# Performance work log

Hardware: AMD Instinct MI355X
Metric: run time of the kernel (lower is better)

The kernel has to match this reference:

```python
import jax, jax.numpy as jnp
import numpy as np

N = 65536      # total nodes = B * MAXN
E = 524288     # edges (avg degree 8)
DX = 32; DG = 32
IN_DIM = DX + 3 * DG   # 128, after concat(x, g0, g1, g2)
H = 256; OUT = 8; MAXN = 8192


def setup_inputs() -> dict:
    key = jax.random.key(0)
    ks = jax.random.split(key, 40)
    inp = {}
    inp['x'] = jax.random.normal(ks[0], (N, DX), jnp.float32)
    inp['g0'] = jax.random.normal(ks[1], (N, DG), jnp.float32)
    inp['g1'] = jax.random.normal(ks[2], (N, DG), jnp.float32)
    inp['g2'] = jax.random.normal(ks[3], (N, DG), jnp.float32)
    inp['edge_src'] = jax.random.randint(ks[4], (E,), 0, N, jnp.int32)
    inp['edge_dst'] = jax.random.randint(ks[5], (E,), 0, N, jnp.int32)
    dims = [(IN_DIM, H), (H, H), (H, H), (H, H)]
    k = 6
    for i, (di, do) in enumerate(dims):
        s = 1.0 / np.sqrt(di)
        inp[f'Wl{i}'] = jax.random.uniform(ks[k], (di, do), jnp.float32, -s, s); k += 1
        inp[f'Wr{i}'] = jax.random.uniform(ks[k], (di, do), jnp.float32, -s, s); k += 1
        inp[f'b{i}'] = jnp.zeros((do,), jnp.float32)
    s = 1.0 / np.sqrt(MAXN)
    inp['mlp1_W1'] = jax.random.uniform(ks[k], (MAXN, H), jnp.float32, -s, s); k += 1
    inp['mlp1_b1'] = jnp.zeros((H,), jnp.float32)
    s = 1.0 / np.sqrt(H)
    inp['mlp1_W2'] = jax.random.uniform(ks[k], (H, 1), jnp.float32, -s, s); k += 1
    inp['mlp1_b2'] = jnp.zeros((1,), jnp.float32)
    inp['bn_gamma'] = jnp.ones((H,), jnp.float32)
    inp['bn_beta'] = jnp.zeros((H,), jnp.float32)
    inp['mlp2_W1'] = jax.random.uniform(ks[k], (H, H), jnp.float32, -s, s); k += 1
    inp['mlp2_b1'] = jnp.zeros((H,), jnp.float32)
    inp['mlp2_W2'] = jax.random.uniform(ks[k], (H, OUT), jnp.float32, -s, s); k += 1
    inp['mlp2_b2'] = jnp.zeros((OUT,), jnp.float32)
    return inp


def _forward(x, g0, g1, g2, edge_src, edge_dst,
             Wl0, Wr0, b0, Wl1, Wr1, b1, Wl2, Wr2, b2, Wl3, Wr3, b3,
             mlp1_W1, mlp1_b1, mlp1_W2, mlp1_b2, bn_gamma, bn_beta,
             mlp2_W1, mlp2_b1, mlp2_W2, mlp2_b2):
    h = jnp.concatenate([x, g0, g1, g2], axis=1)  # [N, IN_DIM]
    # mean-aggregation denominator (in-degree, clamped at 1 like PyG mean)
    cnt = jnp.maximum(
        jax.ops.segment_sum(jnp.ones((E,), h.dtype), edge_dst, num_segments=N), 1.0)
    for Wl, Wr, b in ((Wl0, Wr0, b0), (Wl1, Wr1, b1), (Wl2, Wr2, b2), (Wl3, Wr3, b3)):
        agg = jax.ops.segment_sum(h[edge_src], edge_dst, num_segments=N) / cnt[:, None]
        # SAGEConv: lin_l(mean of neighbors) + lin_r(self) + bias, then ReLU
        h = jax.nn.relu(agg @ Wl + h @ Wr + b)
        # F.dropout in eval / deterministic reference: identity
    h = h.reshape(-1, H, MAXN)                               # [B, H, MAXN]
    h = jax.nn.relu(jnp.einsum('bhm,mk->bhk', h, mlp1_W1) + mlp1_b1)
    h = (jnp.einsum('bhk,ko->bho', h, mlp1_W2) + mlp1_b2)[..., 0]  # [B, H]
    mean = h.mean(axis=0)
    var = h.var(axis=0)
    h = (h - mean) / jnp.sqrt(var + 1e-5) * bn_gamma + bn_beta
    h = jax.nn.relu(h)
    h = jax.nn.relu(h @ mlp2_W1 + mlp2_b1)
    return h @ mlp2_W2 + mlp2_b2                              # [B, OUT]


def reference(x, g0, g1, g2, edge_src, edge_dst,
              Wl0, Wr0, b0, Wl1, Wr1, b1, Wl2, Wr2, b2, Wl3, Wr3, b3,
              mlp1_W1, mlp1_b1, mlp1_W2, mlp1_b2, bn_gamma, bn_beta,
              mlp2_W1, mlp2_b1, mlp2_W2, mlp2_b2):
    return _forward(x, g0, g1, g2, edge_src, edge_dst,
                    Wl0, Wr0, b0, Wl1, Wr1, b1, Wl2, Wr2, b2, Wl3, Wr3, b3,
                    mlp1_W1, mlp1_b1, mlp1_W2, mlp1_b2, bn_gamma, bn_beta,
                    mlp2_W1, mlp2_b1, mlp2_W2, mlp2_b2)
```

## Files before the change

### kernel.cpp

```cpp
#include <hip/hip_runtime.h>
#include <hip/hip_bf16.h>


#define NN 65536
#define EE 524288
#define ROWS 65537
#define PCSR_CAP 720896

using frag16 = __attribute__((ext_vector_type(8))) short;
using f32x4  = __attribute__((ext_vector_type(4))) float;

__device__ __forceinline__ float b2f(unsigned short u) {
    union { unsigned u32; float f; } x; x.u32 = (unsigned)u << 16; return x.f;
}

__device__ __forceinline__ unsigned short f2b(float f) {
    return (unsigned short)(__bfloat16_as_ushort(__float2bfloat16(f)));
}

__device__ __forceinline__ void gld_lds16(const void* g, void* l) {
    __builtin_amdgcn_global_load_lds(
        (const __attribute__((address_space(1))) void*)g,
        (__attribute__((address_space(3))) void*)l, 16, 0, 0);
}


__global__ void gs_zero_deg(int* deg) {
    int i = blockIdx.x * 256 + threadIdx.x;
    if (i < NN) deg[i] = 0;
}

__global__ void gs_hist(const int* __restrict__ dst, int* __restrict__ deg) {
    int e = blockIdx.x * 256 + threadIdx.x;
    atomicAdd(&deg[dst[e]], 1);
}

__global__ void gs_deg_reduce(const int* __restrict__ deg, int* __restrict__ bsum) {
    int t = threadIdx.x;
    int p = (deg[blockIdx.x * 256 + t] + 3) & ~3;
#pragma unroll
    for (int off = 32; off > 0; off >>= 1) p += __shfl_down(p, off);
    __shared__ int w4[4];
    if ((t & 63) == 0) w4[t >> 6] = p;
    __syncthreads();
    if (t == 0) bsum[blockIdx.x] = w4[0] + w4[1] + w4[2] + w4[3];
}

__global__ void gs_scan_bsum(const int* __restrict__ bsum, int* __restrict__ bofs,
                             int* __restrict__ prow) {
    __shared__ int part[256];
    int t = threadIdx.x;
    int v = bsum[t];
    part[t] = v;
    __syncthreads();
    for (int off = 1; off < 256; off <<= 1) {
        int add = (t >= off) ? part[t - off] : 0;
        __syncthreads();
        part[t] += add;
        __syncthreads();
    }
    bofs[t] = part[t] - v;
    if (t == 255) prow[NN] = part[255];
}

__global__ void gs_scan_apply(const int* __restrict__ deg, const int* __restrict__ bofs,
                              int* __restrict__ prow, int* __restrict__ cursor,
                              float* __restrict__ inv_cnt, int* __restrict__ pcsr,
                              __hip_bfloat16* __restrict__ P0,
                              __hip_bfloat16* __restrict__ P1) {
    __shared__ int part[256];
    int t = threadIdx.x;
    int i = blockIdx.x * 256 + t;
    int d = deg[i];
    int p = (d + 3) & ~3;
    part[t] = p;
    __syncthreads();
    for (int off = 1; off < 256; off <<= 1) {
        int add = (t >= off) ? part[t - off] : 0;
        __syncthreads();
        part[t] += add;
        __syncthreads();
    }
    int beg = bofs[blockIdx.x] + part[t] - p;
    prow[i] = beg;
    cursor[i] = beg;
    inv_cnt[i] = 1.0f / (float)(d > 0 ? d : 1);
    for (int j = d; j < p; ++j) pcsr[beg + j] = NN;
    if (blockIdx.x == 0) {
        ((unsigned*)(P0 + (size_t)NN * 512))[t] = 0u;
        ((unsigned*)(P1 + (size_t)NN * 512))[t] = 0u;
    }
}

__global__ void gs_bucket(const int* __restrict__ src, const int* __restrict__ dst,
                          int* __restrict__ cursor, int* __restrict__ pcsr) {
    int e = blockIdx.x * 256 + threadIdx.x;
    int d = dst[e];
    int p = atomicAdd(&cursor[d], 1);
    pcsr[p] = src[e];
}

struct TcvtArgs {
    const float* src[8];
    __hip_bfloat16* dst[8];
    int ldk[8];
    int kofs[8];
    int kblk[8];
};

__global__ void gs_tcvt_all(TcvtArgs a) {
    int z = blockIdx.z;
    if ((int)blockIdx.x >= a.kblk[z]) return;
    const float* src = a.src[z];
    __hip_bfloat16* dst = a.dst[z];
    int ldk = a.ldk[z], kofs = a.kofs[z];
    __shared__ float tile[32][33];
    int kb = blockIdx.x * 32, nb = blockIdx.y * 32;
    int tx = threadIdx.x, ty = threadIdx.y;
#pragma unroll
    for (int i = 0; i < 32; i += 8)
        tile[ty + i][tx] = src[(size_t)(kb + ty + i) * 256 + nb + tx];
    __syncthreads();
#pragma unroll
    for (int i = 0; i < 32; i += 8) {
        int n = nb + ty + i, k = kb + tx;
        dst[(size_t)n * ldk + kofs + k] = __float2bfloat16(tile[tx][ty + i]);
    }
}

__global__ void gs_tcvt(const float* __restrict__ src, __hip_bfloat16* __restrict__ dst,
                        int ldk, int kofs) {
    __shared__ float tile[32][33];
    int kb = blockIdx.x * 32, nb = blockIdx.y * 32;
    int tx = threadIdx.x, ty = threadIdx.y;
#pragma unroll
    for (int i = 0; i < 32; i += 8)
        tile[ty + i][tx] = src[(size_t)(kb + ty + i) * 256 + nb + tx];
    __syncthreads();
#pragma unroll
    for (int i = 0; i < 32; i += 8) {
        int n = nb + ty + i, k = kb + tx;
        dst[(size_t)n * ldk + kofs + k] = __float2bfloat16(tile[tx][ty + i]);
    }
}

__global__ void gs_concat_bf(const float* __restrict__ x, const float* __restrict__ g0,
                             const float* __restrict__ g1, const float* __restrict__ g2,
                             __hip_bfloat16* __restrict__ h) {
    int idx = blockIdx.x * 256 + threadIdx.x;
    int n = idx >> 7, c = idx & 127;
    float v;
    if (c < 32)       v = x[n * 32 + c];
    else if (c < 64)  v = g0[n * 32 + (c - 32)];
    else if (c < 96)  v = g1[n * 32 + (c - 64)];
    else              v = g2[n * 32 + (c - 96)];
    h[(size_t)n * 512 + 256 + c] = __float2bfloat16(v);
}

template <int DIM>
__global__ void gs_agg_bf(const __hip_bfloat16* __restrict__ hsrc,
                          __hip_bfloat16* __restrict__ adst,
                          const int* __restrict__ prow, const int* __restrict__ pcsr,
                          const float* __restrict__ inv_cnt) {
    int wave = threadIdx.x >> 6;
    int lane = threadIdx.x & 63;
    int n = blockIdx.x * 4 + wave;
    int e = prow[n], pe = prow[n + 1];
    float iv = inv_cnt[n];
    if constexpr (DIM == 256) {
        const __hip_bfloat16* base = hsrc + lane * 4;
        float a0 = 0.f, a1 = 0.f, a2 = 0.f, a3 = 0.f;
        while (e < pe) {
            int4 ia = *(const int4*)(pcsr + e);
            int4 ib;
            if (e + 4 < pe) ib = *(const int4*)(pcsr + e + 4);
            else            ib = make_int4(NN, NN, NN, NN);
            e += 8;
            ushort4 v0 = *(const ushort4*)(base + (size_t)ia.x * 512);
            ushort4 v1 = *(const ushort4*)(base + (size_t)ia.y * 512);
            ushort4 v2 = *(const ushort4*)(base + (size_t)ia.z * 512);
            ushort4 v3 = *(const ushort4*)(base + (size_t)ia.w * 512);
            ushort4 v4 = *(const ushort4*)(base + (size_t)ib.x * 512);
            ushort4 v5 = *(const ushort4*)(base + (size_t)ib.y * 512);
            ushort4 v6 = *(const ushort4*)(base + (size_t)ib.z * 512);
            ushort4 v7 = *(const ushort4*)(base + (size_t)ib.w * 512);
            a0 += b2f(v0.x); a1 += b2f(v0.y); a2 += b2f(v0.z); a3 += b2f(v0.w);
            a0 += b2f(v1.x); a1 += b2f(v1.y); a2 += b2f(v1.z); a3 += b2f(v1.w);
            a0 += b2f(v2.x); a1 += b2f(v2.y); a2 += b2f(v2.z); a3 += b2f(v2.w);
            a0 += b2f(v3.x); a1 += b2f(v3.y); a2 += b2f(v3.z); a3 += b2f(v3.w);
            a0 += b2f(v4.x); a1 += b2f(v4.y); a2 += b2f(v4.z); a3 += b2f(v4.w);
            a0 += b2f(v5.x); a1 += b2f(v5.y); a2 += b2f(v5.z); a3 += b2f(v5.w);
            a0 += b2f(v6.x); a1 += b2f(v6.y); a2 += b2f(v6.z); a3 += b2f(v6.w);
            a0 += b2f(v7.x); a1 += b2f(v7.y); a2 += b2f(v7.z); a3 += b2f(v7.w);
        }
        __hip_bfloat16 o[4] = {__float2bfloat16(a0 * iv), __float2bfloat16(a1 * iv),
                               __float2bfloat16(a2 * iv), __float2bfloat16(a3 * iv)};
        *(ushort4*)(adst + (size_t)n * 512 + lane * 4) = *(const ushort4*)o;
    } else {
        const __hip_bfloat16* base = hsrc + lane * 2;
        float a0 = 0.f, a1 = 0.f;
        while (e < pe) {
            int4 ia = *(const int4*)(pcsr + e);
            int4 ib;
            if (e + 4 < pe) ib = *(const int4*)(pcsr + e + 4);
            else            ib = make_int4(NN, NN, NN, NN);
            e += 8;
            ushort2 v0 = *(const ushort2*)(base + (size_t)ia.x * 512);
            ushort2 v1 = *(const ushort2*)(base + (size_t)ia.y * 512);
            ushort2 v2 = *(const ushort2*)(base + (size_t)ia.z * 512);
            ushort2 v3 = *(const ushort2*)(base + (size_t)ia.w * 512);
            ushort2 v4 = *(const ushort2*)(base + (size_t)ib.x * 512);
            ushort2 v5 = *(const ushort2*)(base + (size_t)ib.y * 512);
            ushort2 v6 = *(const ushort2*)(base + (size_t)ib.z * 512);
            ushort2 v7 = *(const ushort2*)(base + (size_t)ib.w * 512);
            a0 += b2f(v0.x); a1 += b2f(v0.y);
            a0 += b2f(v1.x); a1 += b2f(v1.y);
            a0 += b2f(v2.x); a1 += b2f(v2.y);
            a0 += b2f(v3.x); a1 += b2f(v3.y);
            a0 += b2f(v4.x); a1 += b2f(v4.y);
            a0 += b2f(v5.x); a1 += b2f(v5.y);
            a0 += b2f(v6.x); a1 += b2f(v6.y);
            a0 += b2f(v7.x); a1 += b2f(v7.y);
        }
        __hip_bfloat16 o[2] = {__float2bfloat16(a0 * iv), __float2bfloat16(a1 * iv)};
        *(ushort2*)(adst + (size_t)n * 512 + lane * 2) = *(const ushort2*)o;
    }
}

__device__ __forceinline__ void mfma_block(const __hip_bfloat16* A, int lda,
                                           const __hip_bfloat16* Bt, int ldb,
                                           int kbeg, int kend, size_t row0, size_t nbase,
                                           __hip_bfloat16* As, __hip_bfloat16* Bs,
                                           f32x4 acc[4][4]) {
    const int t = threadIdx.x;
    const int lane = t & 63;
    const int w = t >> 6;
    const int wr = (w >> 1) * 64;
    const int wc = (w & 1) * 64;
    const int srow = w * 32 + (lane >> 3);
    const int scol = (lane & 7) * 8;
    for (int kc = kbeg; kc < kend; kc += 64) {
#pragma unroll
        for (int l = 0; l < 4; ++l) {
            gld_lds16(A + (row0 + srow + 8 * l) * (size_t)lda + kc + scol,
                      As + (w * 32 + 8 * l) * 64);
            gld_lds16(Bt + (nbase + srow + 8 * l) * (size_t)ldb + kc + scol,
                      Bs + (w * 32 + 8 * l) * 64);
        }
        __syncthreads();
#pragma unroll
        for (int kk = 0; kk < 64; kk += 32) {
            frag16 af[4], bf[4];
#pragma unroll
            for (int i = 0; i < 4; ++i)
                af[i] = *(const frag16*)(As + (wr + i * 16 + (lane & 15)) * 64 + kk + (lane >> 4) * 8);
#pragma unroll
            for (int j = 0; j < 4; ++j)
                bf[j] = *(const frag16*)(Bs + (wc + j * 16 + (lane & 15)) * 64 + kk + (lane >> 4) * 8);
#pragma unroll
            for (int i = 0; i < 4; ++i)
#pragma unroll
                for (int j = 0; j < 4; ++j)
                    acc[i][j] = __builtin_amdgcn_mfma_f32_16x16x32_bf16(bf[j], af[i], acc[i][j], 0, 0, 0);
        }
        __syncthreads();
    }
}

__global__ __launch_bounds__(256, 2)
void gs_gemm_bias_relu(const __hip_bfloat16* __restrict__ A, int lda, int K,
                       const __hip_bfloat16* __restrict__ Bt, int ldb,
                       const float* __restrict__ bias,
                       __hip_bfloat16* __restrict__ C, int ldc, int cofs) {
    __shared__ __hip_bfloat16 As[128 * 64];
    __shared__ __hip_bfloat16 Bs[128 * 64];
    f32x4 acc[4][4] = {};
    const size_t row0 = (size_t)blockIdx.x * 128;
    const size_t nbase = (size_t)blockIdx.y * 128;
    mfma_block(A, lda, Bt, ldb, 0, K, row0, nbase, As, Bs, acc);
    const int lane = threadIdx.x & 63;
    const int w = threadIdx.x >> 6;
    const int wr = (w >> 1) * 64, wc = (w & 1) * 64;
#pragma unroll
    for (int j = 0; j < 4; ++j) {
        int nb = wc + j * 16 + (lane >> 4) * 4;
        const float4 bv = *(const float4*)&bias[(int)nbase + nb];
#pragma unroll
        for (int i = 0; i < 4; ++i) {
            int m = wr + i * 16 + (lane & 15);
            unsigned short o[4];
            o[0] = f2b(fmaxf(acc[i][j][0] + bv.x, 0.f));
            o[1] = f2b(fmaxf(acc[i][j][1] + bv.y, 0.f));
            o[2] = f2b(fmaxf(acc[i][j][2] + bv.z, 0.f));
            o[3] = f2b(fmaxf(acc[i][j][3] + bv.w, 0.f));
            *(ushort4*)(C + (row0 + m) * (size_t)ldc + cofs + nbase + nb) = *(const ushort4*)o;
        }
    }
}

__global__ __launch_bounds__(256, 2)
void gs_gemm_splitk(const __hip_bfloat16* __restrict__ A, int lda,
                    const __hip_bfloat16* __restrict__ Bt, int ldb,
                    float* __restrict__ part) {
    __shared__ __hip_bfloat16 As[128 * 64];
    __shared__ __hip_bfloat16 Bs[128 * 64];
    f32x4 acc[4][4] = {};
    const size_t row0 = (size_t)blockIdx.x * 128;
    const size_t nbase = (size_t)blockIdx.y * 128;
    const int kbeg = blockIdx.z * 1024;
    mfma_block(A, lda, Bt, ldb, kbeg, kbeg + 1024, row0, nbase, As, Bs, acc);
    const int lane = threadIdx.x & 63;
    const int w = threadIdx.x >> 6;
    const int wr = (w >> 1) * 64, wc = (w & 1) * 64;
    float* p = part + (size_t)blockIdx.z * 2048 * 256;
#pragma unroll
    for (int j = 0; j < 4; ++j) {
        int nb = wc + j * 16 + (lane >> 4) * 4;
#pragma unroll
        for (int i = 0; i < 4; ++i) {
            int m = wr + i * 16 + (lane & 15);
            *(f32x4*)(p + (row0 + m) * 256 + nbase + nb) = acc[i][j];
        }
    }
}

__global__ void gs_mlp1_reduce(const float* __restrict__ part, const float* __restrict__ b1,
                               float* __restrict__ t1) {
    int idx = blockIdx.x * 256 + threadIdx.x;
    float s = 0.f;
#pragma unroll
    for (int ks = 0; ks < 8; ++ks) s += part[(size_t)ks * 524288 + idx];
    s += b1[idx & 255];
    t1[idx] = fmaxf(s, 0.f);
}

__global__ void gs_pool(const float* __restrict__ t1, const float* __restrict__ W2,
                        const float* __restrict__ b2, float* __restrict__ pooled) {
    int r = blockIdx.x;
    int l = threadIdx.x;
    float acc = 0.f;
#pragma unroll
    for (int q = 0; q < 4; ++q) {
        int c = l + q * 64;
        acc = fmaf(t1[(size_t)r * 256 + c], W2[c], acc);
    }
    for (int off = 32; off > 0; off >>= 1) acc += __shfl_down(acc, off);
    if (l == 0) pooled[r] = acc + b2[0];
}

__global__ void gs_bn_mlp2(const float* __restrict__ pooled, const float* __restrict__ gamma,
                           const float* __restrict__ beta, const float* __restrict__ W1,
                           const float* __restrict__ b1, const float* __restrict__ W2,
                           const float* __restrict__ b2, float* __restrict__ out) {
    __shared__ float hb[8][256];
    __shared__ float h2[8][256];
    int t = threadIdx.x;
    {
        float v[8];
        float m = 0.f;
#pragma unroll
        for (int b = 0; b < 8; ++b) { v[b] = pooled[b * 256 + t]; m += v[b]; }
        m *= 0.125f;
        float var = 0.f;
#pragma unroll
        for (int b = 0; b < 8; ++b) { float d = v[b] - m; var += d * d; }
        var *= 0.125f;
        float is = 1.0f / sqrtf(var + 1e-5f);
        float g = gamma[t], bt = beta[t];
#pragma unroll
        for (int b = 0; b < 8; ++b) hb[b][t] = fmaxf((v[b] - m) * is * g + bt, 0.f);
    }
    __syncthreads();
    {
        float acc[8] = {};
        for (int i = 0; i < 256; ++i) {
            float w = W1[i * 256 + t];
#pragma unroll
            for (int b = 0; b < 8; ++b) acc[b] = fmaf(hb[b][i], w, acc[b]);
        }
        float bb = b1[t];
#pragma unroll
        for (int b = 0; b < 8; ++b) h2[b][t] = fmaxf(acc[b] + bb, 0.f);
    }
    __syncthreads();
    if (t < 64) {
        int b = t >> 3, o = t & 7;
        float acc = 0.f;
        for (int j = 0; j < 256; ++j) acc = fmaf(h2[b][j], W2[j * 8 + o], acc);
        out[b * 8 + o] = acc + b2[o];
    }
}

extern "C" void kernel_launch(void* const* d_in, const int* in_sizes, int n_in,
                              void* d_out, int out_size, void* d_ws, size_t ws_size,
                              hipStream_t stream) {
    const float* x  = (const float*)d_in[0];
    const float* g0 = (const float*)d_in[1];
    const float* g1 = (const float*)d_in[2];
    const float* g2 = (const float*)d_in[3];
    const int* edge_src = (const int*)d_in[4];
    const int* edge_dst = (const int*)d_in[5];
    const float* Wl[4] = {(const float*)d_in[6], (const float*)d_in[9],
                          (const float*)d_in[12], (const float*)d_in[15]};
    const float* Wr[4] = {(const float*)d_in[7], (const float*)d_in[10],
                          (const float*)d_in[13], (const float*)d_in[16]};
    const float* bs[4] = {(const float*)d_in[8], (const float*)d_in[11],
                          (const float*)d_in[14], (const float*)d_in[17]};
    const float* mlp1_W1 = (const float*)d_in[18];
    const float* mlp1_b1 = (const float*)d_in[19];
    const float* mlp1_W2 = (const float*)d_in[20];
    const float* mlp1_b2 = (const float*)d_in[21];
    const float* bn_gamma = (const float*)d_in[22];
    const float* bn_beta  = (const float*)d_in[23];
    const float* mlp2_W1 = (const float*)d_in[24];
    const float* mlp2_b1 = (const float*)d_in[25];
    const float* mlp2_W2 = (const float*)d_in[26];
    const float* mlp2_b2 = (const float*)d_in[27];
    float* out = (float*)d_out;

    char* ws = (char*)d_ws;
    __hip_bfloat16* P0 = (__hip_bfloat16*)ws;
    __hip_bfloat16* P1 = P0 + (size_t)ROWS * 512;
    __hip_bfloat16* WC0 = P1 + (size_t)ROWS * 512;
    __hip_bfloat16* WC1 = WC0 + 65536;
    __hip_bfloat16* WC2 = WC1 + 131072;
    __hip_bfloat16* WC3 = WC2 + 131072;
    __hip_bfloat16* W1T = WC3 + 131072;
    float* inv_cnt = (float*)(W1T + 2097152);
    int* ideg = (int*)(inv_cnt + 65536);
    int* prow = ideg + 65536;
    int* cursor = prow + 65544;
    int* bsum = cursor + 65536;
    int* bofs = bsum + 256;
    int* pcsr = bofs + 256;
    __hip_bfloat16* H4 = P0;
    float* T1 = (float*)P1;
    float* pooled = T1 + 524288;
    float* PART = (float*)((char*)P1 + (size_t)(4 << 20));

    gs_zero_deg<<<256, 256, 0, stream>>>(ideg);
    gs_hist<<<EE / 256, 256, 0, stream>>>(edge_dst, ideg);
    gs_deg_reduce<<<256, 256, 0, stream>>>(ideg, bsum);
    gs_scan_bsum<<<1, 256, 0, stream>>>(bsum, bofs, prow);
    gs_scan_apply<<<256, 256, 0, stream>>>(ideg, bofs, prow, cursor, inv_cnt, pcsr, P0, P1);
    gs_bucket<<<EE / 256, 256, 0, stream>>>(edge_src, edge_dst, cursor, pcsr);

    {
        TcvtArgs a;
        const float* srcs[8] = {Wl[0], Wr[0], Wl[1], Wr[1], Wl[2], Wr[2], Wl[3], Wr[3]};
        __hip_bfloat16* dsts[8] = {WC0, WC0, WC1, WC1, WC2, WC2, WC3, WC3};
        int ldks[8] = {256, 256, 512, 512, 512, 512, 512, 512};
        int kofss[8] = {0, 128, 0, 256, 0, 256, 0, 256};
        int kblks[8] = {4, 4, 8, 8, 8, 8, 8, 8};
        for (int i = 0; i < 8; ++i) {
            a.src[i] = srcs[i]; a.dst[i] = dsts[i];
            a.ldk[i] = ldks[i]; a.kofs[i] = kofss[i]; a.kblk[i] = kblks[i];
        }
        gs_tcvt_all<<<dim3(8, 8, 8), dim3(32, 8), 0, stream>>>(a);
    }
    gs_tcvt<<<dim3(256, 8), dim3(32, 8), 0, stream>>>(mlp1_W1, W1T, 8192, 0);

    gs_concat_bf<<<NN * 128 / 256, 256, 0, stream>>>(x, g0, g1, g2, P0);

    gs_agg_bf<128><<<NN / 4, 256, 0, stream>>>(P0 + 256, P0 + 128, prow, pcsr, inv_cnt);
    gs_gemm_bias_relu<<<dim3(NN / 128, 2), 256, 0, stream>>>(P0 + 128, 512, 256, WC0, 256,
                                                             bs[0], P1, 512, 256);
    gs_agg_bf<256><<<NN / 4, 256, 0, stream>>>(P1 + 256, P1, prow, pcsr, inv_cnt);
    gs_gemm_bias_relu<<<dim3(NN / 128, 2), 256, 0, stream>>>(P1, 512, 512, WC1, 512,
                                                             bs[1], P0, 512, 256);
    gs_agg_bf<256><<<NN / 4, 256, 0, stream>>>(P0 + 256, P0, prow, pcsr, inv_cnt);
    gs_gemm_bias_relu<<<dim3(NN / 128, 2), 256, 0, stream>>>(P0, 512, 512, WC2, 512,
                                                             bs[2], P1, 512, 256);
    gs_agg_bf<256><<<NN / 4, 256, 0, stream>>>(P1 + 256, P1, prow, pcsr, inv_cnt);
    gs_gemm_bias_relu<<<dim3(NN / 128, 2), 256, 0, stream>>>(P1, 512, 512, WC3, 512,
                                                             bs[3], H4, 256, 0);

    gs_gemm_splitk<<<dim3(16, 2, 8), 256, 0, stream>>>(H4, 8192, W1T, 8192, PART);
    gs_mlp1_reduce<<<2048, 256, 0, stream>>>(PART, mlp1_b1, T1);
    gs_pool<<<2048, 64, 0, stream>>>(T1, mlp1_W2, mlp1_b2, pooled);

    gs_bn_mlp2<<<1, 256, 0, stream>>>(pooled, bn_gamma, bn_beta, mlp2_W1, mlp2_b1,
                                      mlp2_W2, mlp2_b2, out);
}
```

Before: 531.8 us.

## Widen GEMM tiles to full N=256, pad CSR to 8, fuse mlp1 reduce and pool

The GEMMs now use 128x256 output tiles per block, so the A tile is loaded once instead of twice across two column blocks. The split-K GEMM goes from 8 to 16 K-splits to keep enough blocks in flight. CSR rows are padded to multiples of 8 so the aggregation loop can prefetch the next 8 neighbor indices without bounds checks, at the cost of more dummy gathers. The mlp1 reduce and pooling kernels are fused so the T1 intermediate is never written, though the reduce now reads twice as many partials and the larger accumulator may raise register pressure.

```diff
diff --git a/kernel.cpp b/kernel.cpp
--- a/kernel.cpp
+++ b/kernel.cpp
@@ -5,7 +5,7 @@
 #define NN 65536
 #define EE 524288
 #define ROWS 65537
-#define PCSR_CAP 720896
+#define PCSR_CAP 983056
 
 using frag16 = __attribute__((ext_vector_type(8))) short;
 using f32x4  = __attribute__((ext_vector_type(4))) float;
@@ -37,7 +37,7 @@
 
 __global__ void gs_deg_reduce(const int* __restrict__ deg, int* __restrict__ bsum) {
     int t = threadIdx.x;
-    int p = (deg[blockIdx.x * 256 + t] + 3) & ~3;
+    int p = (deg[blockIdx.x * 256 + t] + 7) & ~7;
 #pragma unroll
     for (int off = 32; off > 0; off >>= 1) p += __shfl_down(p, off);
     __shared__ int w4[4];
@@ -72,7 +72,7 @@
     int t = threadIdx.x;
     int i = blockIdx.x * 256 + t;
     int d = deg[i];
-    int p = (d + 3) & ~3;
+    int p = (d + 7) & ~7;
     part[t] = p;
     __syncthreads();
     for (int off = 1; off < 256; off <<= 1) {
@@ -89,6 +89,7 @@
     if (blockIdx.x == 0) {
         ((unsigned*)(P0 + (size_t)NN * 512))[t] = 0u;
         ((unsigned*)(P1 + (size_t)NN * 512))[t] = 0u;
+        if (t < 16) pcsr[PCSR_CAP - 16 + t] = NN;
     }
 }
 
@@ -170,20 +171,21 @@
     if constexpr (DIM == 256) {
         const __hip_bfloat16* base = hsrc + lane * 4;
         float a0 = 0.f, a1 = 0.f, a2 = 0.f, a3 = 0.f;
+        int4 ia = *(const int4*)(pcsr + e);
+        int4 ib = *(const int4*)(pcsr + e + 4);
         while (e < pe) {
-            int4 ia = *(const int4*)(pcsr + e);
-            int4 ib;
-            if (e + 4 < pe) ib = *(const int4*)(pcsr + e + 4);
-            else            ib = make_int4(NN, NN, NN, NN);
+            int4 c0 = ia, c1 = ib;
             e += 8;
-            ushort4 v0 = *(const ushort4*)(base + (size_t)ia.x * 512);
-            ushort4 v1 = *(const ushort4*)(base + (size_t)ia.y * 512);
-            ushort4 v2 = *(const ushort4*)(base + (size_t)ia.z * 512);
-            ushort4 v3 = *(const ushort4*)(base + (size_t)ia.w * 512);
-            ushort4 v4 = *(const ushort4*)(base + (size_t)ib.x * 512);
-            ushort4 v5 = *(const ushort4*)(base + (size_t)ib.y * 512);
-            ushort4 v6 = *(const ushort4*)(base + (size_t)ib.z * 512);
-            ushort4 v7 = *(const ushort4*)(base + (size_t)ib.w * 512);
+            ia = *(const int4*)(pcsr + e);
+            ib = *(const int4*)(pcsr + e + 4);
+            ushort4 v0 = *(const ushort4*)(base + (size_t)c0.x * 512);
+            ushort4 v1 = *(const ushort4*)(base + (size_t)c0.y * 512);
+            ushort4 v2 = *(const ushort4*)(base + (size_t)c0.z * 512);
+            ushort4 v3 = *(const ushort4*)(base + (size_t)c0.w * 512);
+            ushort4 v4 = *(const ushort4*)(base + (size_t)c1.x * 512);
+            ushort4 v5 = *(const ushort4*)(base + (size_t)c1.y * 512);
+            ushort4 v6 = *(const ushort4*)(base + (size_t)c1.z * 512);
+            ushort4 v7 = *(const ushort4*)(base + (size_t)c1.w * 512);
             a0 += b2f(v0.x); a1 += b2f(v0.y); a2 += b2f(v0.z); a3 += b2f(v0.w);
             a0 += b2f(v1.x); a1 += b2f(v1.y); a2 += b2f(v1.z); a3 += b2f(v1.w);
             a0 += b2f(v2.x); a1 += b2f(v2.y); a2 += b2f(v2.z); a3 += b2f(v2.w);
@@ -199,20 +201,21 @@
     } else {
         const __hip_bfloat16* base = hsrc + lane * 2;
         float a0 = 0.f, a1 = 0.f;
+        int4 ia = *(const int4*)(pcsr + e);
+        int4 ib = *(const int4*)(pcsr + e + 4);
         while (e < pe) {
-            int4 ia = *(const int4*)(pcsr + e);
-            int4 ib;
-            if (e + 4 < pe) ib = *(const int4*)(pcsr + e + 4);
-            else            ib = make_int4(NN, NN, NN, NN);
+            int4 c0 = ia, c1 = ib;
             e += 8;
-            ushort2 v0 = *(const ushort2*)(base + (size_t)ia.x * 512);
-            ushort2 v1 = *(const ushort2*)(base + (size_t)ia.y * 512);
-            ushort2 v2 = *(const ushort2*)(base + (size_t)ia.z * 512);
-            ushort2 v3 = *(const ushort2*)(base + (size_t)ia.w * 512);
-            ushort2 v4 = *(const ushort2*)(base + (size_t)ib.x * 512);
-            ushort2 v5 = *(const ushort2*)(base + (size_t)ib.y * 512);
-            ushort2 v6 = *(const ushort2*)(base + (size_t)ib.z * 512);
-            ushort2 v7 = *(const ushort2*)(base + (size_t)ib.w * 512);
+            ia = *(const int4*)(pcsr + e);
+            ib = *(const int4*)(pcsr + e + 4);
+            ushort2 v0 = *(const ushort2*)(base + (size_t)c0.x * 512);
+            ushort2 v1 = *(const ushort2*)(base + (size_t)c0.y * 512);
+            ushort2 v2 = *(const ushort2*)(base + (size_t)c0.z * 512);
+            ushort2 v3 = *(const ushort2*)(base + (size_t)c0.w * 512);
+            ushort2 v4 = *(const ushort2*)(base + (size_t)c1.x * 512);
+            ushort2 v5 = *(const ushort2*)(base + (size_t)c1.y * 512);
+            ushort2 v6 = *(const ushort2*)(base + (size_t)c1.z * 512);
+            ushort2 v7 = *(const ushort2*)(base + (size_t)c1.w * 512);
             a0 += b2f(v0.x); a1 += b2f(v0.y);
             a0 += b2f(v1.x); a1 += b2f(v1.y);
             a0 += b2f(v2.x); a1 += b2f(v2.y);
@@ -227,41 +230,41 @@
     }
 }
 
-__device__ __forceinline__ void mfma_block(const __hip_bfloat16* A, int lda,
-                                           const __hip_bfloat16* Bt, int ldb,
-                                           int kbeg, int kend, size_t row0, size_t nbase,
-                                           __hip_bfloat16* As, __hip_bfloat16* Bs,
-                                           f32x4 acc[4][4]) {
+__device__ __forceinline__ void mfma_block_n256(const __hip_bfloat16* A, int lda,
+                                                const __hip_bfloat16* Bt, int ldb,
+                                                int kbeg, int kend, size_t row0,
+                                                __hip_bfloat16* As, __hip_bfloat16* Bs,
+                                                f32x4 acc[4][8]) {
     const int t = threadIdx.x;
     const int lane = t & 63;
     const int w = t >> 6;
     const int wr = (w >> 1) * 64;
-    const int wc = (w & 1) * 64;
-    const int srow = w * 32 + (lane >> 3);
+    const int wc = (w & 1) * 128;
+    const int sr8 = lane >> 3;
     const int scol = (lane & 7) * 8;
     for (int kc = kbeg; kc < kend; kc += 64) {
 #pragma unroll
-        for (int l = 0; l < 4; ++l) {
-            gld_lds16(A + (row0 + srow + 8 * l) * (size_t)lda + kc + scol,
+        for (int l = 0; l < 4; ++l)
+            gld_lds16(A + (row0 + w * 32 + 8 * l + sr8) * (size_t)lda + kc + scol,
                       As + (w * 32 + 8 * l) * 64);
-            gld_lds16(Bt + (nbase + srow + 8 * l) * (size_t)ldb + kc + scol,
-                      Bs + (w * 32 + 8 * l) * 64);
-        }
+#pragma unroll
+        for (int l = 0; l < 8; ++l)
+            gld_lds16(Bt + (size_t)(w * 64 + 8 * l + sr8) * ldb + kc + scol,
+                      Bs + (w * 64 + 8 * l) * 64);
         __syncthreads();
 #pragma unroll
         for (int kk = 0; kk < 64; kk += 32) {
-            frag16 af[4], bf[4];
+            frag16 af[4];
 #pragma unroll
             for (int i = 0; i < 4; ++i)
                 af[i] = *(const frag16*)(As + (wr + i * 16 + (lane & 15)) * 64 + kk + (lane >> 4) * 8);
 #pragma unroll
-            for (int j = 0; j < 4; ++j)
-                bf[j] = *(const frag16*)(Bs + (wc + j * 16 + (lane & 15)) * 64 + kk + (lane >> 4) * 8);
-#pragma unroll
-            for (int i = 0; i < 4; ++i)
-#pragma unroll
-                for (int j = 0; j < 4; ++j)
-                    acc[i][j] = __builtin_amdgcn_mfma_f32_16x16x32_bf16(bf[j], af[i], acc[i][j], 0, 0, 0);
+            for (int j = 0; j < 8; ++j) {
+                frag16 bf = *(const frag16*)(Bs + (wc + j * 16 + (lane & 15)) * 64 + kk + (lane >> 4) * 8);
+#pragma unroll
+                for (int i = 0; i < 4; ++i)
+                    acc[i][j] = __builtin_amdgcn_mfma_f32_16x16x32_bf16(bf, af[i], acc[i][j], 0, 0, 0);
+            }
         }
         __syncthreads();
     }
@@ -273,18 +276,17 @@
                        const float* __restrict__ bias,
                        __hip_bfloat16* __restrict__ C, int ldc, int cofs) {
     __shared__ __hip_bfloat16 As[128 * 64];
-    __shared__ __hip_bfloat16 Bs[128 * 64];
-    f32x4 acc[4][4] = {};
+    __shared__ __hip_bfloat16 Bs[256 * 64];
+    f32x4 acc[4][8] = {};
     const size_t row0 = (size_t)blockIdx.x * 128;
-    const size_t nbase = (size_t)blockIdx.y * 128;
-    mfma_block(A, lda, Bt, ldb, 0, K, row0, nbase, As, Bs, acc);
+    mfma_block_n256(A, lda, Bt, ldb, 0, K, row0, As, Bs, acc);
     const int lane = threadIdx.x & 63;
     const int w = threadIdx.x >> 6;
-    const int wr = (w >> 1) * 64, wc = (w & 1) * 64;
-#pragma unroll
-    for (int j = 0; j < 4; ++j) {
+    const int wr = (w >> 1) * 64, wc = (w & 1) * 128;
+#pragma unroll
+    for (int j = 0; j < 8; ++j) {
         int nb = wc + j * 16 + (lane >> 4) * 4;
-        const float4 bv = *(const float4*)&bias[(int)nbase + nb];
+        const float4 bv = *(const float4*)&bias[nb];
 #pragma unroll
         for (int i = 0; i < 4; ++i) {
             int m = wr + i * 16 + (lane & 15);
@@ -293,7 +295,7 @@
             o[1] = f2b(fmaxf(acc[i][j][1] + bv.y, 0.f));
             o[2] = f2b(fmaxf(acc[i][j][2] + bv.z, 0.f));
             o[3] = f2b(fmaxf(acc[i][j][3] + bv.w, 0.f));
-            *(ushort4*)(C + (row0 + m) * (size_t)ldc + cofs + nbase + nb) = *(const ushort4*)o;
+            *(ushort4*)(C + (row0 + m) * (size_t)ldc + cofs + nb) = *(const ushort4*)o;
         }
     }
 }
@@ -303,49 +305,44 @@
                     const __hip_bfloat16* __restrict__ Bt, int ldb,
                     float* __restrict__ part) {
     __shared__ __hip_bfloat16 As[128 * 64];
-    __shared__ __hip_bfloat16 Bs[128 * 64];
-    f32x4 acc[4][4] = {};
+    __shared__ __hip_bfloat16 Bs[256 * 64];
+    f32x4 acc[4][8] = {};
     const size_t row0 = (size_t)blockIdx.x * 128;
-    const size_t nbase = (size_t)blockIdx.y * 128;
-    const int kbeg = blockIdx.z * 1024;
-    mfma_block(A, lda, Bt, ldb, kbeg, kbeg + 1024, row0, nbase, As, Bs, acc);
+    const int kbeg = blockIdx.y * 512;
+    mfma_block_n256(A, lda, Bt, ldb, kbeg, kbeg + 512, row0, As, Bs, acc);
     const int lane = threadIdx.x & 63;
     const int w = threadIdx.x >> 6;
-    const int wr = (w >> 1) * 64, wc = (w & 1) * 64;
-    float* p = part + (size_t)blockIdx.z * 2048 * 256;
-#pragma unroll
-    for (int j = 0; j < 4; ++j) {
+    const int wr = (w >> 1) * 64, wc = (w & 1) * 128;
+    float* p = part + (size_t)blockIdx.y * 2048 * 256;
+#pragma unroll
+    for (int j = 0; j < 8; ++j) {
         int nb = wc + j * 16 + (lane >> 4) * 4;
 #pragma unroll
         for (int i = 0; i < 4; ++i) {
             int m = wr + i * 16 + (lane & 15);
-            *(f32x4*)(p + (row0 + m) * 256 + nbase + nb) = acc[i][j];
-        }
-    }
-}
-
-__global__ void gs_mlp1_reduce(const float* __restrict__ part, const float* __restrict__ b1,
-                               float* __restrict__ t1) {
-    int idx = blockIdx.x * 256 + threadIdx.x;
+            *(f32x4*)(p + (row0 + m) * 256 + nb) = acc[i][j];
+        }
+    }
+}
+
+__global__ void gs_mlp1_reduce_pool(const float* __restrict__ part,
+                                    const float* __restrict__ b1,
+                                    const float* __restrict__ W2,
+                                    const float* __restrict__ b2,
+                                    float* __restrict__ pooled) {
+    __shared__ float w4[4];
+    int r = blockIdx.x;
+    int t = threadIdx.x;
+    size_t idx = (size_t)r * 256 + t;
     float s = 0.f;
 #pragma unroll
-    for (int ks = 0; ks < 8; ++ks) s += part[(size_t)ks * 524288 + idx];
-    s += b1[idx & 255];
-    t1[idx] = fmaxf(s, 0.f);
-}
-
-__global__ void gs_pool(const float* __restrict__ t1, const float* __restrict__ W2,
-                        const float* __restrict__ b2, float* __restrict__ pooled) {
-    int r = blockIdx.x;
-    int l = threadIdx.x;
-    float acc = 0.f;
-#pragma unroll
-    for (int q = 0; q < 4; ++q) {
-        int c = l + q * 64;
-        acc = fmaf(t1[(size_t)r * 256 + c], W2[c], acc);
-    }
-    for (int off = 32; off > 0; off >>= 1) acc += __shfl_down(acc, off);
-    if (l == 0) pooled[r] = acc + b2[0];
+    for (int ks = 0; ks < 16; ++ks) s += part[(size_t)ks * 524288 + idx];
+    s = fmaxf(s + b1[t], 0.f) * W2[t];
+#pragma unroll
+    for (int off = 32; off > 0; off >>= 1) s += __shfl_down(s, off);
+    if ((t & 63) == 0) w4[t >> 6] = s;
+    __syncthreads();
+    if (t == 0) pooled[r] = w4[0] + w4[1] + w4[2] + w4[3] + b2[0];
 }
 
 __global__ void gs_bn_mlp2(const float* __restrict__ pooled, const float* __restrict__ gamma,
@@ -434,8 +431,7 @@
     int* bofs = bsum + 256;
     int* pcsr = bofs + 256;
     __hip_bfloat16* H4 = P0;
-    float* T1 = (float*)P1;
-    float* pooled = T1 + 524288;
+    float* pooled = (float*)((char*)P1 + (size_t)(2 << 20));
     float* PART = (float*)((char*)P1 + (size_t)(4 << 20));
 
     gs_zero_deg<<<256, 256, 0, stream>>>(ideg);
@@ -463,21 +459,20 @@
     gs_concat_bf<<<NN * 128 / 256, 256, 0, stream>>>(x, g0, g1, g2, P0);
 
     gs_agg_bf<128><<<NN / 4, 256, 0, stream>>>(P0 + 256, P0 + 128, prow, pcsr, inv_cnt);
-    gs_gemm_bias_relu<<<dim3(NN / 128, 2), 256, 0, stream>>>(P0 + 128, 512, 256, WC0, 256,
-                                                             bs[0], P1, 512, 256);
+    gs_gemm_bias_relu<<<NN / 128, 256, 0, stream>>>(P0 + 128, 512, 256, WC0, 256,
+                                                    bs[0], P1, 512, 256);
     gs_agg_bf<256><<<NN / 4, 256, 0, stream>>>(P1 + 256, P1, prow, pcsr, inv_cnt);
-    gs_gemm_bias_relu<<<dim3(NN / 128, 2), 256, 0, stream>>>(P1, 512, 512, WC1, 512,
-                                                             bs[1], P0, 512, 256);
+    gs_gemm_bias_relu<<<NN / 128, 256, 0, stream>>>(P1, 512, 512, WC1, 512,
+                                                    bs[1], P0, 512, 256);
     gs_agg_bf<256><<<NN / 4, 256, 0, stream>>>(P0 + 256, P0, prow, pcsr, inv_cnt);
-    gs_gemm_bias_relu<<<dim3(NN / 128, 2), 256, 0, stream>>>(P0, 512, 512, WC2, 512,
-                                                             bs[2], P1, 512, 256);
+    gs_gemm_bias_relu<<<NN / 128, 256, 0, stream>>>(P0, 512, 512, WC2, 512,
+                                                    bs[2], P1, 512, 256);
     gs_agg_bf<256><<<NN / 4, 256, 0, stream>>>(P1 + 256, P1, prow, pcsr, inv_cnt);
-    gs_gemm_bias_relu<<<dim3(NN / 128, 2), 256, 0, stream>>>(P1, 512, 512, WC3, 512,
-                                                             bs[3], H4, 256, 0);
-
-    gs_gemm_splitk<<<dim3(16, 2, 8), 256, 0, stream>>>(H4, 8192, W1T, 8192, PART);
-    gs_mlp1_reduce<<<2048, 256, 0, stream>>>(PART, mlp1_b1, T1);
-    gs_pool<<<2048, 64, 0, stream>>>(T1, mlp1_W2, mlp1_b2, pooled);
+    gs_gemm_bias_relu<<<NN / 128, 256, 0, stream>>>(P1, 512, 512, WC3, 512,
+                                                    bs[3], H4, 256, 0);
+
+    gs_gemm_splitk<<<dim3(16, 16), 256, 0, stream>>>(H4, 8192, W1T, 8192, PART);
+    gs_mlp1_reduce_pool<<<2048, 256, 0, stream>>>(PART, mlp1_b1, mlp1_W2, mlp1_b2, pooled);
 
     gs_bn_mlp2<<<1, 256, 0, stream>>>(pooled, bn_gamma, bn_beta, mlp2_W1, mlp2_b1,
                                       mlp2_W2, mlp2_b2, out);
```

Measured after the change: 531.1 us. About the same (-0.1%).
